# Kernel tuning notes

Hardware: AMD Instinct MI355X
Metric: run time of the kernel (lower is better)

The kernel has to match this reference:

```python
import jax, jax.numpy as jnp
import numpy as np

NUM_ITERS = 3

def squash(s, axis=-1):
    # standard capsule squash: ||s||^2/(1+||s||^2) * s/||s||
    sq = jnp.sum(s * s, axis=axis, keepdims=True)
    norm = jnp.sqrt(sq)
    return (sq / (1.0 + sq)) * (s / norm)

def setup_inputs() -> dict:
    key = jax.random.key(0)
    kx, kw = jax.random.split(key)
    B, I, k, l, O = 512, 1152, 8, 16, 7
    x = jax.random.normal(kx, (B, I, k), dtype=jnp.float32)
    w = jax.random.normal(kw, (I, k, l, O), dtype=jnp.float32)
    return {"x": x, "w": w}

def reference(x, w):
    # x: [B, I, k]; w: [I, k, l, O]
    u_hat = jnp.einsum('BIk,IklO->BIlO', x, w)            # [B, I, l, O]
    I, _, l, _ = w.shape
    b_ij = jnp.zeros((I, l), dtype=u_hat.dtype)
    v_j = None
    for _ in range(NUM_ITERS):
        c_ij = jax.nn.softmax(b_ij, axis=0)               # softmax over I
        s_j = jnp.einsum('Il,BIlO->BlO', c_ij, u_hat)     # [B, l, O]
        v_j = jnp.transpose(squash(s_j), (0, 2, 1))       # [B, O, l]
        u_vj = jnp.einsum('BOl,BIlO->BIl', v_j, u_hat).mean(axis=0)  # [I, l]
        b_ij = b_ij + u_vj
    return v_j
```

## Files before the change

kernel.cpp:

```cpp
#include <hip/hip_runtime.h>
#include <hip/hip_bf16.h>


#define NB 512
#define NI 1152
#define NLO 112
#define NIK 9216
#define KSPLIT 48
#define SPART 57344

typedef __attribute__((ext_vector_type(8))) short bf16x8;
typedef __attribute__((ext_vector_type(4))) float f32x4;

__device__ __forceinline__ ushort f2bf(float f) {
    __hip_bfloat16 h = __float2bfloat16(f);
    return *(ushort*)&h;
}

__global__ void softmax_col(const float* __restrict__ b, float* __restrict__ c) {
    int l = blockIdx.x;
    int t = threadIdx.x;
    __shared__ float red[256];
    float m = -1e30f;
    for (int i = t; i < NI; i += 256) m = fmaxf(m, b[i * 16 + l]);
    red[t] = m; __syncthreads();
    for (int s = 128; s > 0; s >>= 1) {
        if (t < s) red[t] = fmaxf(red[t], red[t + s]);
        __syncthreads();
    }
    m = red[0]; __syncthreads();
    float sum = 0.f;
    for (int i = t; i < NI; i += 256) sum += expf(b[i * 16 + l] - m);
    red[t] = sum; __syncthreads();
    for (int s = 128; s > 0; s >>= 1) {
        if (t < s) red[t] += red[t + s];
        __syncthreads();
    }
    float inv = 1.0f / red[0];
    for (int i = t; i < NI; i += 256) c[i * 16 + l] = expf(b[i * 16 + l] - m) * inv;
}

__global__ __launch_bounds__(256) void conv_x(const float* __restrict__ x,
                                              ushort* __restrict__ xbf,
                                              ushort* __restrict__ xT) {
    __shared__ ushort tile[64][68];
    int kg = blockIdx.x % 144, bg = blockIdx.x / 144;
    int k0 = kg * 64, b0 = bg * 64;
    int t = threadIdx.x;
    for (int e = t; e < 1024; e += 256) {
        int r = e >> 4, c4 = (e & 15) * 4;
        float4 f = *(const float4*)&x[(size_t)(b0 + r) * NIK + k0 + c4];
        ushort4 u = { f2bf(f.x), f2bf(f.y), f2bf(f.z), f2bf(f.w) };
        *(ushort4*)&xbf[(size_t)(b0 + r) * NIK + k0 + c4] = u;
        tile[r][c4] = u.x; tile[r][c4 + 1] = u.y; tile[r][c4 + 2] = u.z; tile[r][c4 + 3] = u.w;
    }
    __syncthreads();
    for (int e = t; e < 1024; e += 256) {
        int kr = e >> 4, c4 = (e & 15) * 4;
        ushort4 u = { tile[c4][kr], tile[c4 + 1][kr], tile[c4 + 2][kr], tile[c4 + 3][kr] };
        *(ushort4*)&xT[(size_t)(k0 + kr) * NB + b0 + c4] = u;
    }
}

__global__ __launch_bounds__(256) void conv_wc(const float* __restrict__ c,
                                               const float* __restrict__ w,
                                               ushort* __restrict__ wcT) {
    __shared__ ushort tile[NLO][66];
    __shared__ float cs[128];
    int ik0 = blockIdx.x * 64;
    int t = threadIdx.x;
    if (t < 128) cs[t] = c[(size_t)(ik0 >> 3) * 16 + t];
    __syncthreads();
    for (int e = t; e < 7168; e += 256) {
        int ikl = e / NLO, lo = e - ikl * NLO;
        int il = ((ikl >> 3) << 4) + lo / 7;
        tile[lo][ikl] = f2bf(cs[il] * w[(size_t)(ik0 + ikl) * NLO + lo]);
    }
    __syncthreads();
    for (int e = t; e < 7168; e += 256) {
        int lo = e >> 6, ikl = e & 63;
        wcT[(size_t)lo * NIK + ik0 + ikl] = tile[lo][ikl];
    }
}

__global__ __launch_bounds__(256) void s_gemm(const ushort* __restrict__ xbf,
                                              const ushort* __restrict__ wcT,
                                              float* __restrict__ part) {
    int wid = blockIdx.x * 4 + (threadIdx.x >> 6);
    int lane = threadIdx.x & 63;
    int mt = wid & 31;
    int kc = wid >> 5;
    int b0 = mt * 16, k0 = kc * 192;
    int row = lane & 15, quad = lane >> 4;
    const ushort* ap = xbf + (size_t)(b0 + row) * NIK + k0 + quad * 8;
    const ushort* bp = wcT + (size_t)row * NIK + k0 + quad * 8;
    f32x4 acc[7];
    #pragma unroll
    for (int nt = 0; nt < 7; ++nt) acc[nt] = (f32x4){0.f, 0.f, 0.f, 0.f};
    for (int ks = 0; ks < 6; ++ks) {
        bf16x8 a = *(const bf16x8*)(ap + ks * 32);
        #pragma unroll
        for (int nt = 0; nt < 7; ++nt) {
            bf16x8 bfr = *(const bf16x8*)(bp + (size_t)nt * 16 * NIK + ks * 32);
            acc[nt] = __builtin_amdgcn_mfma_f32_16x16x32_bf16(a, bfr, acc[nt], 0, 0, 0);
        }
    }
    float* pp = part + (size_t)kc * SPART + (size_t)(b0 + quad * 4) * NLO + row;
    #pragma unroll
    for (int nt = 0; nt < 7; ++nt)
        #pragma unroll
        for (int r = 0; r < 4; ++r)
            pp[(size_t)r * NLO + nt * 16] = acc[nt][r];
}

__global__ void squash_k(const float* __restrict__ part, ushort* __restrict__ vT,
                         float* __restrict__ out, int write_out) {
    int b = blockIdx.x;
    int t = threadIdx.x;
    __shared__ float sh[NLO];
    __shared__ float fac[16];
    float sv = 0.f;
    if (t < NLO) {
        const float* p = part + (size_t)b * NLO + t;
        #pragma unroll 8
        for (int kc = 0; kc < KSPLIT; ++kc) sv += p[(size_t)kc * SPART];
        sh[t] = sv;
    }
    __syncthreads();
    if (t < 16) {
        float sq = 0.f;
        #pragma unroll
        for (int o = 0; o < 7; ++o) { float e = sh[t * 7 + o]; sq += e * e; }
        fac[t] = sqrtf(sq) / (1.0f + sq);
    }
    __syncthreads();
    if (t < NLO) {
        int l = t / 7, o = t - l * 7;
        float vv = sv * fac[l];
        vT[(size_t)(o * 16 + l) * NB + b] = f2bf(vv);
        if (write_out) out[(size_t)b * NLO + o * 16 + l] = vv;
    }
}

__global__ __launch_bounds__(256) void g_fused(const ushort* __restrict__ xT,
                                               const ushort* __restrict__ vT,
                                               const float* __restrict__ w,
                                               float* __restrict__ bij) {
    int wid = blockIdx.x * 4 + (threadIdx.x >> 6);
    int lane = threadIdx.x & 63;
    int m0 = wid * 16;
    int row = lane & 15, quad = lane >> 4;
    const ushort* ap = xT + (size_t)(m0 + row) * NB + quad * 8;
    const ushort* bp = vT + (size_t)row * NB + quad * 8;
    f32x4 acc[7];
    #pragma unroll
    for (int nt = 0; nt < 7; ++nt) acc[nt] = (f32x4){0.f, 0.f, 0.f, 0.f};
    for (int ks = 0; ks < 16; ++ks) {
        bf16x8 a = *(const bf16x8*)(ap + ks * 32);
        #pragma unroll
        for (int nt = 0; nt < 7; ++nt) {
            bf16x8 bfr = *(const bf16x8*)(bp + (size_t)nt * 16 * NB + ks * 32);
            acc[nt] = __builtin_amdgcn_mfma_f32_16x16x32_bf16(a, bfr, acc[nt], 0, 0, 0);
        }
    }
    float S = 0.f;
    #pragma unroll
    for (int r = 0; r < 4; ++r) {
        int ik = m0 + quad * 4 + r;
        const float* wr = w + (size_t)ik * NLO + row * 7;
        float p = 0.f;
        #pragma unroll
        for (int o = 0; o < 7; ++o) p += wr[o] * acc[o][r];
        S += p;
    }
    float Sp = __shfl_down(S, 16);
    if ((quad & 1) == 0) {
        int i = (m0 >> 3) + (quad >> 1);
        bij[(size_t)i * 16 + row] += (S + Sp) * (1.0f / 512.0f);
    }
}

extern "C" void kernel_launch(void* const* d_in, const int* in_sizes, int n_in,
                              void* d_out, int out_size, void* d_ws, size_t ws_size,
                              hipStream_t stream) {
    const float* x = (const float*)d_in[0];
    const float* w = (const float*)d_in[1];
    float* out = (float*)d_out;
    float* ws = (float*)d_ws;
    float*  f_b    = ws;
    float*  f_c    = f_b + 18432;
    float*  f_part = f_c + 18432;
    ushort* xbf    = (ushort*)(f_part + (size_t)KSPLIT * SPART);
    ushort* xT     = xbf + (size_t)NB * NIK;
    ushort* wcT    = xT + (size_t)NIK * NB;
    ushort* vT     = wcT + (size_t)NLO * NIK;
    hipMemsetAsync(f_b, 0, 18432 * sizeof(float), stream);
    conv_x<<<1152, 256, 0, stream>>>(x, xbf, xT);
    for (int it = 0; it < 3; ++it) {
        softmax_col<<<16, 256, 0, stream>>>(f_b, f_c);
        conv_wc<<<144, 256, 0, stream>>>(f_c, w, wcT);
        s_gemm<<<384, 256, 0, stream>>>(xbf, wcT, f_part);
        squash_k<<<512, 128, 0, stream>>>(f_part, vT, out, it == 2 ? 1 : 0);
        if (it < 2) g_fused<<<144, 256, 0, stream>>>(xT, vT, w, f_b);
    }
}
```

Measured before the change: 199.8 us.

## Double split-K parallelism, split agreement GEMM over batch, skip first softmax

Doubles the split-K factor in the s GEMM (768 blocks, 3 k-steps each) and splits the agreement GEMM over two batch halves that write separate partial b_ij buffers, which softmax then sums. The first iteration skips the softmax and memset by using the uniform coefficient 1/1152 directly. Both GEMMs now fully unroll their k loops. The aim is more blocks in flight on a wide GPU and fewer tiny launches, paid for with twice the partial-sum traffic that squash_k must reduce.

```diff
diff --git a/kernel.cpp b/kernel.cpp
--- a/kernel.cpp
+++ b/kernel.cpp
@@ -6,7 +6,7 @@
 #define NI 1152
 #define NLO 112
 #define NIK 9216
-#define KSPLIT 48
+#define KSPLIT 96
 #define SPART 57344
 
 typedef __attribute__((ext_vector_type(8))) short bf16x8;
@@ -15,29 +15,6 @@
 __device__ __forceinline__ ushort f2bf(float f) {
     __hip_bfloat16 h = __float2bfloat16(f);
     return *(ushort*)&h;
-}
-
-__global__ void softmax_col(const float* __restrict__ b, float* __restrict__ c) {
-    int l = blockIdx.x;
-    int t = threadIdx.x;
-    __shared__ float red[256];
-    float m = -1e30f;
-    for (int i = t; i < NI; i += 256) m = fmaxf(m, b[i * 16 + l]);
-    red[t] = m; __syncthreads();
-    for (int s = 128; s > 0; s >>= 1) {
-        if (t < s) red[t] = fmaxf(red[t], red[t + s]);
-        __syncthreads();
-    }
-    m = red[0]; __syncthreads();
-    float sum = 0.f;
-    for (int i = t; i < NI; i += 256) sum += expf(b[i * 16 + l] - m);
-    red[t] = sum; __syncthreads();
-    for (int s = 128; s > 0; s >>= 1) {
-        if (t < s) red[t] += red[t + s];
-        __syncthreads();
-    }
-    float inv = 1.0f / red[0];
-    for (int i = t; i < NI; i += 256) c[i * 16 + l] = expf(b[i * 16 + l] - m) * inv;
 }
 
 __global__ __launch_bounds__(256) void conv_x(const float* __restrict__ x,
@@ -62,14 +39,40 @@
     }
 }
 
+__global__ void softmax_col(const float* __restrict__ bijp, float* __restrict__ c) {
+    const float* b0 = bijp;
+    const float* b1 = bijp + NI * 16;
+    int l = blockIdx.x;
+    int t = threadIdx.x;
+    __shared__ float red[256];
+    float m = -1e30f;
+    for (int i = t; i < NI; i += 256) m = fmaxf(m, b0[i * 16 + l] + b1[i * 16 + l]);
+    red[t] = m; __syncthreads();
+    for (int s = 128; s > 0; s >>= 1) {
+        if (t < s) red[t] = fmaxf(red[t], red[t + s]);
+        __syncthreads();
+    }
+    m = red[0]; __syncthreads();
+    float sum = 0.f;
+    for (int i = t; i < NI; i += 256) sum += expf(b0[i * 16 + l] + b1[i * 16 + l] - m);
+    red[t] = sum; __syncthreads();
+    for (int s = 128; s > 0; s >>= 1) {
+        if (t < s) red[t] += red[t + s];
+        __syncthreads();
+    }
+    float inv = 1.0f / red[0];
+    for (int i = t; i < NI; i += 256)
+        c[i * 16 + l] = expf(b0[i * 16 + l] + b1[i * 16 + l] - m) * inv;
+}
+
 __global__ __launch_bounds__(256) void conv_wc(const float* __restrict__ c,
                                                const float* __restrict__ w,
-                                               ushort* __restrict__ wcT) {
+                                               ushort* __restrict__ wcT, int it0) {
     __shared__ ushort tile[NLO][66];
     __shared__ float cs[128];
     int ik0 = blockIdx.x * 64;
     int t = threadIdx.x;
-    if (t < 128) cs[t] = c[(size_t)(ik0 >> 3) * 16 + t];
+    if (t < 128) cs[t] = it0 ? (1.0f / 1152.0f) : c[(size_t)(ik0 >> 3) * 16 + t];
     __syncthreads();
     for (int e = t; e < 7168; e += 256) {
         int ikl = e / NLO, lo = e - ikl * NLO;
@@ -90,14 +93,15 @@
     int lane = threadIdx.x & 63;
     int mt = wid & 31;
     int kc = wid >> 5;
-    int b0 = mt * 16, k0 = kc * 192;
+    int b0 = mt * 16, k0 = kc * 96;
     int row = lane & 15, quad = lane >> 4;
     const ushort* ap = xbf + (size_t)(b0 + row) * NIK + k0 + quad * 8;
     const ushort* bp = wcT + (size_t)row * NIK + k0 + quad * 8;
     f32x4 acc[7];
     #pragma unroll
     for (int nt = 0; nt < 7; ++nt) acc[nt] = (f32x4){0.f, 0.f, 0.f, 0.f};
-    for (int ks = 0; ks < 6; ++ks) {
+    #pragma unroll
+    for (int ks = 0; ks < 3; ++ks) {
         bf16x8 a = *(const bf16x8*)(ap + ks * 32);
         #pragma unroll
         for (int nt = 0; nt < 7; ++nt) {
@@ -145,17 +149,20 @@
 __global__ __launch_bounds__(256) void g_fused(const ushort* __restrict__ xT,
                                                const ushort* __restrict__ vT,
                                                const float* __restrict__ w,
-                                               float* __restrict__ bij) {
+                                               float* __restrict__ bijp, int accum) {
     int wid = blockIdx.x * 4 + (threadIdx.x >> 6);
     int lane = threadIdx.x & 63;
-    int m0 = wid * 16;
+    int half = wid & 1;
+    int m0 = (wid >> 1) * 16;
+    int kb0 = half * 256;
     int row = lane & 15, quad = lane >> 4;
-    const ushort* ap = xT + (size_t)(m0 + row) * NB + quad * 8;
-    const ushort* bp = vT + (size_t)row * NB + quad * 8;
+    const ushort* ap = xT + (size_t)(m0 + row) * NB + kb0 + quad * 8;
+    const ushort* bp = vT + (size_t)row * NB + kb0 + quad * 8;
     f32x4 acc[7];
     #pragma unroll
     for (int nt = 0; nt < 7; ++nt) acc[nt] = (f32x4){0.f, 0.f, 0.f, 0.f};
-    for (int ks = 0; ks < 16; ++ks) {
+    #pragma unroll
+    for (int ks = 0; ks < 8; ++ks) {
         bf16x8 a = *(const bf16x8*)(ap + ks * 32);
         #pragma unroll
         for (int nt = 0; nt < 7; ++nt) {
@@ -176,7 +183,9 @@
     float Sp = __shfl_down(S, 16);
     if ((quad & 1) == 0) {
         int i = (m0 >> 3) + (quad >> 1);
-        bij[(size_t)i * 16 + row] += (S + Sp) * (1.0f / 512.0f);
+        float val = (S + Sp) * (1.0f / 512.0f);
+        float* dst = bijp + (size_t)half * (NI * 16) + i * 16 + row;
+        *dst = accum ? (*dst + val) : val;
     }
 }
 
@@ -187,20 +196,19 @@
     const float* w = (const float*)d_in[1];
     float* out = (float*)d_out;
     float* ws = (float*)d_ws;
-    float*  f_b    = ws;
-    float*  f_c    = f_b + 18432;
+    float*  f_bijp = ws;
+    float*  f_c    = f_bijp + 2 * NI * 16;
     float*  f_part = f_c + 18432;
     ushort* xbf    = (ushort*)(f_part + (size_t)KSPLIT * SPART);
     ushort* xT     = xbf + (size_t)NB * NIK;
     ushort* wcT    = xT + (size_t)NIK * NB;
     ushort* vT     = wcT + (size_t)NLO * NIK;
-    hipMemsetAsync(f_b, 0, 18432 * sizeof(float), stream);
     conv_x<<<1152, 256, 0, stream>>>(x, xbf, xT);
     for (int it = 0; it < 3; ++it) {
-        softmax_col<<<16, 256, 0, stream>>>(f_b, f_c);
-        conv_wc<<<144, 256, 0, stream>>>(f_c, w, wcT);
-        s_gemm<<<384, 256, 0, stream>>>(xbf, wcT, f_part);
+        if (it > 0) softmax_col<<<16, 256, 0, stream>>>(f_bijp, f_c);
+        conv_wc<<<144, 256, 0, stream>>>(f_c, w, wcT, it == 0 ? 1 : 0);
+        s_gemm<<<768, 256, 0, stream>>>(xbf, wcT, f_part);
         squash_k<<<512, 128, 0, stream>>>(f_part, vT, out, it == 2 ? 1 : 0);
-        if (it < 2) g_fused<<<144, 256, 0, stream>>>(xT, vT, w, f_b);
-    }
-}
+        if (it < 2) g_fused<<<288, 256, 0, stream>>>(xT, vT, w, f_bijp, it);
+    }
+}
```

After: 201.7 us. Within noise of the previous version (+0.9%).
